# Kernel tuning notes

Measured on AMD Instinct MI355X. Metric: run time of the kernel, lower is better.

The kernel has to match this reference:

```python
import jax, jax.numpy as jnp
import numpy as np

B, N, H = 8, 1024, 32


def _mlp(x, W1, b1, W2, b2, W3, b3):
    # Normalization(mean=0, std=1) is identity; leaky_relu slope 0.01 (torch default)
    h = jax.nn.leaky_relu(x @ W1 + b1)
    h = jax.nn.leaky_relu(h @ W2 + b2)
    return jnp.tanh(h @ W3 + b3)


def setup_inputs() -> dict:
    key = jax.random.key(0)
    ks = jax.random.split(key, 10)
    s = 0.1  # small init scale for numerical sanity under tanh
    return {
        "x": jax.random.normal(ks[0], (B, N, 2), dtype=jnp.float32),
        "A": jax.random.uniform(ks[1], (N, N), dtype=jnp.float32),
        "Wm1": jax.random.normal(ks[2], (2, H), dtype=jnp.float32) * s,
        "bm1": jnp.zeros((H,), jnp.float32),
        "Wm2": jax.random.normal(ks[3], (H, H), dtype=jnp.float32) * s,
        "bm2": jnp.zeros((H,), jnp.float32),
        "Wm3": jax.random.normal(ks[4], (H, 1), dtype=jnp.float32) * s,
        "bm3": jnp.zeros((1,), jnp.float32),
        "Wx1": jax.random.normal(ks[5], (2, H), dtype=jnp.float32) * s,
        "bx1": jnp.zeros((H,), jnp.float32),
        "Wx2": jax.random.normal(ks[6], (H, H), dtype=jnp.float32) * s,
        "bx2": jnp.zeros((H,), jnp.float32),
        "Wx3": jax.random.normal(ks[7], (H, 1), dtype=jnp.float32) * s,
        "bx3": jnp.zeros((1,), jnp.float32),
    }


def reference(x, A, Wm1, bm1, Wm2, bm2, Wm3, bm3, Wx1, bx1, Wx2, bx2, Wx3, bx3):
    rho = x[:, :, 0]  # [B, N]
    V = x[:, :, 1]    # [B, N]
    # pairwise message: message[b, i, j] = (rho[b,i]+rho[b,j], V[b,i]+V[b,j])
    msg = jnp.stack(
        [rho[:, None, :] + rho[:, :, None], V[:, None, :] + V[:, :, None]],
        axis=-1,
    )  # [B, N, N, 2]
    me = _mlp(msg, Wm1, bm1, Wm2, bm2, Wm3, bm3)[..., 0]  # [B, N, N]
    msg_sum = jnp.einsum("bij,ij->bi", me, A)  # adjacency-weighted sum over j
    x2 = jnp.stack([rho, msg_sum], axis=-1)  # [B, N, 2]
    return _mlp(x2, Wx1, bx1, Wx2, bx2, Wx3, bx3)  # [B, N, 1]
```

## Files before the change

kernel.cpp:

```cpp
#include <hip/hip_runtime.h>

#define NB 8
#define NN 1024
#define NH 32

#define FP 99
#define CW 6.0f
#define RW 7.5f
#define UW (CW * RW / (CW + RW))

__device__ __forceinline__ float leaky(float x) { return fmaxf(x, 0.01f * x); }

__device__ __forceinline__ float fast_tanh(float x) {
    float e = __builtin_amdgcn_exp2f(x * 2.88539008177792681f);
    return 1.0f - 2.0f * __builtin_amdgcn_rcpf(1.0f + e);
}

#define SWZ_ADD(v, imm) \
    v += __int_as_float(__builtin_amdgcn_ds_swizzle(__float_as_int(v), imm))

__device__ __forceinline__ unsigned bf16r(float f) {
    unsigned u = __float_as_uint(f);
    return (u + 0x7FFFu + ((u >> 16) & 1u)) >> 16;
}

__device__ __forceinline__ float mlp_me(float s, float t,
    const float* __restrict__ Wm1, const float* __restrict__ bm1,
    const float* __restrict__ Wm2, const float* __restrict__ bm2,
    const float* __restrict__ Wm3, const float* __restrict__ bm3) {
    float h1[NH];
#pragma unroll
    for (int k = 0; k < NH; ++k)
        h1[k] = leaky(s * Wm1[k] + t * Wm1[32 + k] + bm1[k]);
    float acc[NH];
#pragma unroll
    for (int h = 0; h < NH; ++h) acc[h] = bm2[h];
#pragma unroll
    for (int k = 0; k < NH; ++k) {
#pragma unroll
        for (int h4 = 0; h4 < 8; ++h4) {
            const float4 wv = *(const float4*)(Wm2 + k * 32 + h4 * 4);
            acc[h4 * 4 + 0] = fmaf(h1[k], wv.x, acc[h4 * 4 + 0]);
            acc[h4 * 4 + 1] = fmaf(h1[k], wv.y, acc[h4 * 4 + 1]);
            acc[h4 * 4 + 2] = fmaf(h1[k], wv.z, acc[h4 * 4 + 2]);
            acc[h4 * 4 + 3] = fmaf(h1[k], wv.w, acc[h4 * 4 + 3]);
        }
    }
    float z = bm3[0];
#pragma unroll
    for (int h = 0; h < NH; ++h) z = fmaf(leaky(acc[h]), Wm3[h], z);
    return fast_tanh(z);
}

__global__ __launch_bounds__(256) void table_kernel(
    const float* __restrict__ Wm1, const float* __restrict__ bm1,
    const float* __restrict__ Wm2, const float* __restrict__ bm2,
    const float* __restrict__ Wm3, const float* __restrict__ bm3,
    uint2* __restrict__ tq) {
    const int gid = blockIdx.x * 256 + threadIdx.x;
    if (gid >= FP * FP) return;
    const int iy = gid / FP;
    const int ix = gid - iy * FP;
    if (ix >= FP - 1 || iy >= FP - 1) { tq[gid] = make_uint2(0u, 0u); return; }

    const float hu = 2.0f * UW / (float)(FP - 1);
    auto unwarp = [](float u) { return u / (1.0f - fabsf(u) / CW); };
    const float s0 = unwarp(fmaf((float)ix, hu, -UW));
    const float s1 = unwarp(fmaf((float)(ix + 1), hu, -UW));
    const float t0 = unwarp(fmaf((float)iy, hu, -UW));
    const float t1 = unwarp(fmaf((float)(iy + 1), hu, -UW));

    const float f00 = mlp_me(s0, t0, Wm1, bm1, Wm2, bm2, Wm3, bm3);
    const float f10 = mlp_me(s1, t0, Wm1, bm1, Wm2, bm2, Wm3, bm3);
    const float f01 = mlp_me(s0, t1, Wm1, bm1, Wm2, bm2, Wm3, bm3);

    uint2 cell;
    cell.x = __float_as_uint(f00);
    cell.y = bf16r(f10 - f00) | (bf16r(f01 - f00) << 16);
    tq[gid] = cell;
}

__global__ __launch_bounds__(1024, 8) void edge_out_kernel(
    const float* __restrict__ x, const float* __restrict__ A,
    const uint2* __restrict__ tq,
    const float* __restrict__ Wx1, const float* __restrict__ bx1,
    const float* __restrict__ Wx2, const float* __restrict__ bx2,
    const float* __restrict__ Wx3, const float* __restrict__ bx3,
    float* __restrict__ out) {
    __shared__ uint2 sfq[FP * FP];

    const int tid = threadIdx.x;
    {
        const float4* __restrict__ src = (const float4*)tq;
        float4* dst = (float4*)sfq;
        for (int idx = tid; idx < (FP * FP) / 2; idx += 1024) dst[idx] = src[idx];
        if (tid == 0) sfq[FP * FP - 1] = tq[FP * FP - 1];
    }
    __syncthreads();

    const int wave = tid >> 6;
    const int lane = tid & 63;
    const int w    = blockIdx.x * 16 + wave;
    const int i    = w >> 3;
    const int b    = w & 7;
    const int node = b * NN + i;

    const float2 xi = ((const float2*)x)[node];
    const float4* __restrict__ xb4 = (const float4*)((const float2*)x + b * NN);
    const float2* __restrict__ Ar2 = (const float2*)(A + (size_t)i * NN);

    const float hu     = 2.0f * UW / (float)(FP - 1);
    const float inv_hu = 1.0f / hu;
    const float fhi    = (float)(FP - 1) - 0.001f;
    const float rcw    = 1.0f / CW;

    float ms0 = 0.0f, ms1 = 0.0f, ms2 = 0.0f, ms3 = 0.0f;
#pragma unroll
    for (int g = 0; g < 2; ++g) {
        float4 xv[4]; float2 av[4];
#pragma unroll
        for (int q = 0; q < 4; ++q) {
            const int p = (g * 4 + q) * 64 + lane;
            xv[q] = xb4[p];
            av[q] = Ar2[p];
        }
        int   idxq[8];
        float asq[8], atq[8];
#pragma unroll
        for (int q = 0; q < 4; ++q) {
#pragma unroll
            for (int e = 0; e < 2; ++e) {
                const float s = xi.x + (e ? xv[q].z : xv[q].x);
                const float t = xi.y + (e ? xv[q].w : xv[q].y);
                const float us = s * __builtin_amdgcn_rcpf(fmaf(fabsf(s), rcw, 1.0f));
                const float ut = t * __builtin_amdgcn_rcpf(fmaf(fabsf(t), rcw, 1.0f));
                const float fs = fminf(fmaxf((us + UW) * inv_hu, 0.0f), fhi);
                const float ft = fminf(fmaxf((ut + UW) * inv_hu, 0.0f), fhi);
                const float fsf = floorf(fs), ftf = floorf(ft);
                asq[q * 2 + e] = fs - fsf;
                atq[q * 2 + e] = ft - ftf;
                idxq[q * 2 + e] = (int)ftf * FP + (int)fsf;
            }
        }
        uint2 cqv[8];
#pragma unroll
        for (int q = 0; q < 8; ++q) cqv[q] = sfq[idxq[q]];
#pragma unroll
        for (int q = 0; q < 8; ++q) {
            const float c00 = __uint_as_float(cqv[q].x);
            const float dcs = __uint_as_float(cqv[q].y << 16);
            const float dct = __uint_as_float(cqv[q].y & 0xFFFF0000u);
            const float me  = fmaf(atq[q], dct, fmaf(asq[q], dcs, c00));
            const float aw  = (q & 1) ? av[q >> 1].y : av[q >> 1].x;
            if      ((q & 3) == 0) ms0 = fmaf(me, aw, ms0);
            else if ((q & 3) == 1) ms1 = fmaf(me, aw, ms1);
            else if ((q & 3) == 2) ms2 = fmaf(me, aw, ms2);
            else                   ms3 = fmaf(me, aw, ms3);
        }
    }
    float msum = (ms0 + ms1) + (ms2 + ms3);

    SWZ_ADD(msum, 0x041F);
    SWZ_ADD(msum, 0x081F);
    SWZ_ADD(msum, 0x101F);
    SWZ_ADD(msum, 0x201F);
    SWZ_ADD(msum, 0x401F);
    msum += __shfl_xor(msum, 32, 64);

    const float rho = xi.x;
    const int h = lane & 31;
    float acc = bx2[h];
#pragma unroll
    for (int k = 0; k < NH; ++k) {
        const float h1k = leaky(fmaf(msum, Wx1[32 + k], fmaf(rho, Wx1[k], bx1[k])));
        acc = fmaf(h1k, Wx2[k * 32 + h], acc);
    }
    float sv = (lane < 32) ? leaky(acc) * Wx3[h] : 0.0f;
    SWZ_ADD(sv, 0x041F);
    SWZ_ADD(sv, 0x081F);
    SWZ_ADD(sv, 0x101F);
    SWZ_ADD(sv, 0x201F);
    SWZ_ADD(sv, 0x401F);
    sv += __shfl_xor(sv, 32, 64);
    if (lane == 0) out[node] = fast_tanh(sv + bx3[0]);
}

extern "C" void kernel_launch(void* const* d_in, const int* in_sizes, int n_in,
                              void* d_out, int out_size, void* d_ws, size_t ws_size,
                              hipStream_t stream) {
    const float* x   = (const float*)d_in[0];
    const float* A   = (const float*)d_in[1];
    const float* Wm1 = (const float*)d_in[2];
    const float* bm1 = (const float*)d_in[3];
    const float* Wm2 = (const float*)d_in[4];
    const float* bm2 = (const float*)d_in[5];
    const float* Wm3 = (const float*)d_in[6];
    const float* bm3 = (const float*)d_in[7];
    const float* Wx1 = (const float*)d_in[8];
    const float* bx1 = (const float*)d_in[9];
    const float* Wx2 = (const float*)d_in[10];
    const float* bx2 = (const float*)d_in[11];
    const float* Wx3 = (const float*)d_in[12];
    const float* bx3 = (const float*)d_in[13];

    uint2* tq  = (uint2*)d_ws;
    float* out = (float*)d_out;

    table_kernel<<<dim3((FP * FP + 255) / 256), dim3(256), 0, stream>>>(
        Wm1, bm1, Wm2, bm2, Wm3, bm3, tq);
    edge_out_kernel<<<dim3(NB * NN / 16), dim3(1024), 0, stream>>>(
        x, A, tq, Wx1, bx1, Wx2, bx2, Wx3, bx3, out);
}
```

Measured before the change: 111.0 us.

## Evaluate MLP table once per grid node, then assemble cells in separate kernel

The table builder used to evaluate the message MLP three times per cell (f00, f10, f01). Now each grid node is evaluated once in its own kernel, with the weights staged in shared memory. A second small kernel then builds the packed base-plus-gradient cells from neighbouring entries. This cuts MLP work in the table build to about a third, at the cost of an extra kernel launch and an intermediate float table in workspace.

```diff
diff --git a/kernel.cpp b/kernel.cpp
--- a/kernel.cpp
+++ b/kernel.cpp
@@ -24,56 +24,68 @@
     return (u + 0x7FFFu + ((u >> 16) & 1u)) >> 16;
 }
 
-__device__ __forceinline__ float mlp_me(float s, float t,
+__global__ __launch_bounds__(256) void eval_kernel(
     const float* __restrict__ Wm1, const float* __restrict__ bm1,
     const float* __restrict__ Wm2, const float* __restrict__ bm2,
-    const float* __restrict__ Wm3, const float* __restrict__ bm3) {
+    const float* __restrict__ Wm3, const float* __restrict__ bm3,
+    float* __restrict__ tabf) {
+    __shared__ __align__(16) float sW2[1024];
+    __shared__ float sW1[64], sb1[32], sb2[32], sW3[32];
+    __shared__ float sb3;
+    const int tid = threadIdx.x;
+#pragma unroll
+    for (int q = 0; q < 4; ++q) sW2[tid + 256 * q] = Wm2[tid + 256 * q];
+    if (tid < 64) sW1[tid] = Wm1[tid];
+    if (tid < 32) { sb1[tid] = bm1[tid]; sb2[tid] = bm2[tid]; sW3[tid] = Wm3[tid]; }
+    if (tid == 0) sb3 = bm3[0];
+    __syncthreads();
+
+    const int gid = blockIdx.x * 256 + tid;
+    if (gid >= FP * FP) return;
+    const int iy = gid / FP;
+    const int ix = gid - iy * FP;
+
+    const float hu = 2.0f * UW / (float)(FP - 1);
+    const float us = fmaf((float)ix, hu, -UW);
+    const float ut = fmaf((float)iy, hu, -UW);
+    const float s = us / (1.0f - fabsf(us) / CW);
+    const float t = ut / (1.0f - fabsf(ut) / CW);
+
     float h1[NH];
 #pragma unroll
     for (int k = 0; k < NH; ++k)
-        h1[k] = leaky(s * Wm1[k] + t * Wm1[32 + k] + bm1[k]);
+        h1[k] = leaky(s * sW1[k] + t * sW1[32 + k] + sb1[k]);
+
     float acc[NH];
 #pragma unroll
-    for (int h = 0; h < NH; ++h) acc[h] = bm2[h];
+    for (int h = 0; h < NH; ++h) acc[h] = sb2[h];
 #pragma unroll
     for (int k = 0; k < NH; ++k) {
 #pragma unroll
         for (int h4 = 0; h4 < 8; ++h4) {
-            const float4 wv = *(const float4*)(Wm2 + k * 32 + h4 * 4);
+            const float4 wv = *(const float4*)(sW2 + k * 32 + h4 * 4);
             acc[h4 * 4 + 0] = fmaf(h1[k], wv.x, acc[h4 * 4 + 0]);
             acc[h4 * 4 + 1] = fmaf(h1[k], wv.y, acc[h4 * 4 + 1]);
             acc[h4 * 4 + 2] = fmaf(h1[k], wv.z, acc[h4 * 4 + 2]);
             acc[h4 * 4 + 3] = fmaf(h1[k], wv.w, acc[h4 * 4 + 3]);
         }
     }
-    float z = bm3[0];
-#pragma unroll
-    for (int h = 0; h < NH; ++h) z = fmaf(leaky(acc[h]), Wm3[h], z);
-    return fast_tanh(z);
-}
-
-__global__ __launch_bounds__(256) void table_kernel(
-    const float* __restrict__ Wm1, const float* __restrict__ bm1,
-    const float* __restrict__ Wm2, const float* __restrict__ bm2,
-    const float* __restrict__ Wm3, const float* __restrict__ bm3,
-    uint2* __restrict__ tq) {
+    float z = sb3;
+#pragma unroll
+    for (int h = 0; h < NH; ++h) z = fmaf(leaky(acc[h]), sW3[h], z);
+    tabf[gid] = fast_tanh(z);
+}
+
+__global__ __launch_bounds__(256) void assemble_kernel(
+    const float* __restrict__ tabf, uint2* __restrict__ tq) {
     const int gid = blockIdx.x * 256 + threadIdx.x;
     if (gid >= FP * FP) return;
     const int iy = gid / FP;
     const int ix = gid - iy * FP;
     if (ix >= FP - 1 || iy >= FP - 1) { tq[gid] = make_uint2(0u, 0u); return; }
-
-    const float hu = 2.0f * UW / (float)(FP - 1);
-    auto unwarp = [](float u) { return u / (1.0f - fabsf(u) / CW); };
-    const float s0 = unwarp(fmaf((float)ix, hu, -UW));
-    const float s1 = unwarp(fmaf((float)(ix + 1), hu, -UW));
-    const float t0 = unwarp(fmaf((float)iy, hu, -UW));
-    const float t1 = unwarp(fmaf((float)(iy + 1), hu, -UW));
-
-    const float f00 = mlp_me(s0, t0, Wm1, bm1, Wm2, bm2, Wm3, bm3);
-    const float f10 = mlp_me(s1, t0, Wm1, bm1, Wm2, bm2, Wm3, bm3);
-    const float f01 = mlp_me(s0, t1, Wm1, bm1, Wm2, bm2, Wm3, bm3);
-
+    const float f00 = tabf[gid];
+    const float f10 = tabf[gid + 1];
+    const float f01 = tabf[gid + FP];
     uint2 cell;
     cell.x = __float_as_uint(f00);
     cell.y = bf16r(f10 - f00) | (bf16r(f01 - f00) << 16);
@@ -203,11 +215,14 @@
     const float* Wx3 = (const float*)d_in[12];
     const float* bx3 = (const float*)d_in[13];
 
-    uint2* tq  = (uint2*)d_ws;
-    float* out = (float*)d_out;
-
-    table_kernel<<<dim3((FP * FP + 255) / 256), dim3(256), 0, stream>>>(
-        Wm1, bm1, Wm2, bm2, Wm3, bm3, tq);
+    uint2* tq   = (uint2*)d_ws;
+    float* tabf = (float*)(tq + FP * FP);
+    float* out  = (float*)d_out;
+
+    const int nblk = (FP * FP + 255) / 256;
+    eval_kernel<<<dim3(nblk), dim3(256), 0, stream>>>(
+        Wm1, bm1, Wm2, bm2, Wm3, bm3, tabf);
+    assemble_kernel<<<dim3(nblk), dim3(256), 0, stream>>>(tabf, tq);
     edge_out_kernel<<<dim3(NB * NN / 16), dim3(1024), 0, stream>>>(
         x, A, tq, Wx1, bx1, Wx2, bx2, Wx3, bx3, out);
 }
```

Measured after the change: 103.6 us. -6.7%, faster.
